# Kernel optimization log

Hardware: AMD Instinct MI355X
Metric: run time of the kernel (lower is better)

The kernel has to match this reference:

```python
import math
import jax, jax.numpy as jnp
import numpy as np
from jax import lax

B, T, D, H, F, K = 4, 1024, 512, 8, 2048, 31
DK = D // H


def _ln(x, g, b, eps=1e-5):
    m = jnp.mean(x, -1, keepdims=True)
    v = jnp.mean((x - m) ** 2, -1, keepdims=True)
    return (x - m) * lax.rsqrt(v + eps) * g + b


def setup_inputs():
    key = jax.random.key(0)
    ks = jax.random.split(key, 16)
    r = lambda k, s: (0.02 * jax.random.normal(k, s)).astype(jnp.float32)
    ones = lambda s: jnp.ones(s, jnp.float32)
    zeros = lambda s: jnp.zeros(s, jnp.float32)
    return {
        'x': jax.random.normal(ks[0], (B, T, D), jnp.float32),
        'pos_k': r(ks[1], (T, T, DK)),
        'mask': jnp.ones((B, T, T), jnp.int32),
        'ffn_in_ln_g': ones((D,)), 'ffn_in_ln_b': zeros((D,)),
        'ffn_in_w1': r(ks[2], (D, F)), 'ffn_in_b1': zeros((F,)),
        'ffn_in_w2': r(ks[3], (F, D)), 'ffn_in_b2': zeros((D,)),
        'attn_ln_g': ones((D,)), 'attn_ln_b': zeros((D,)),
        'wq': r(ks[4], (D, D)), 'bq': zeros((D,)),
        'wk': r(ks[5], (D, D)), 'bk': zeros((D,)),
        'wv': r(ks[6], (D, D)), 'bv': zeros((D,)),
        'wo': r(ks[7], (D, D)), 'bo': zeros((D,)),
        'conv_ln_g': ones((D,)), 'conv_ln_b': zeros((D,)),
        'pw1_w': jnp.asarray([1.0, 1.0], jnp.float32), 'pw1_b': zeros((2,)),
        'dw_w': r(ks[8], (D, 1, K)), 'dw_b': zeros((D,)),
        'pw2_w': jnp.asarray(1.0, jnp.float32), 'pw2_b': jnp.asarray(0.0, jnp.float32),
        'ffn_out_ln_g': ones((D,)), 'ffn_out_ln_b': zeros((D,)),
        'ffn_out_w1': r(ks[9], (D, F)), 'ffn_out_b1': zeros((F,)),
        'ffn_out_w2': r(ks[10], (F, D)), 'ffn_out_b2': zeros((D,)),
        'final_ln_g': ones((D,)), 'final_ln_b': zeros((D,)),
    }


def reference(x, pos_k, mask,
              ffn_in_ln_g, ffn_in_ln_b, ffn_in_w1, ffn_in_b1, ffn_in_w2, ffn_in_b2,
              attn_ln_g, attn_ln_b, wq, bq, wk, bk, wv, bv, wo, bo,
              conv_ln_g, conv_ln_b, pw1_w, pw1_b, dw_w, dw_b, pw2_w, pw2_b,
              ffn_out_ln_g, ffn_out_ln_b, ffn_out_w1, ffn_out_b1, ffn_out_w2, ffn_out_b2,
              final_ln_g, final_ln_b):
    def ffn(z, g, b, w1, b1, w2, b2):
        h = jax.nn.relu(_ln(z, g, b) @ w1 + b1)
        return h @ w2 + b2

    # macaron FFN (half residual)
    x = x + 0.5 * ffn(x, ffn_in_ln_g, ffn_in_ln_b, ffn_in_w1, ffn_in_b1, ffn_in_w2, ffn_in_b2)

    # relative-position multi-head attention (pre-LN)
    y = _ln(x, attn_ln_g, attn_ln_b)
    q = (y @ wq + bq).reshape(B, T, H, DK).transpose(0, 2, 1, 3)  # bhtd
    k = (y @ wk + bk).reshape(B, T, H, DK).transpose(0, 2, 1, 3)
    v = (y @ wv + bv).reshape(B, T, H, DK).transpose(0, 2, 1, 3)
    A = jnp.einsum('bhtd,bhsd->bhts', q, k)
    Bm = jnp.einsum('bhtd,tsd->bhts', q, pos_k)  # rel-pos term
    scores = (A + Bm) / math.sqrt(DK)
    inv = mask[:, None, :, :] == 0  # (B,1,T,T)
    neg = jnp.finfo(scores.dtype).min
    scores = jnp.where(inv, neg, scores)
    attn = jnp.where(inv, 0.0, jax.nn.softmax(scores, axis=-1))
    ctx = jnp.einsum('bhts,bhsd->bhtd', attn, v).transpose(0, 2, 1, 3).reshape(B, T, D)
    x = x + ctx @ wo + bo

    # conv module: LN -> pointwise(1->2) GLU -> depthwise conv1d -> ReLU -> pointwise(1->1)
    y = _ln(x, conv_ln_g, conv_ln_b)
    y = (pw1_w[0] * y + pw1_b[0]) * jax.nn.sigmoid(pw1_w[1] * y + pw1_b[1])
    y = y.transpose(0, 2, 1)  # (B, D, T)
    pad = (K - 1) // 2
    y = lax.conv_general_dilated(y, dw_w, (1,), [(pad, pad)],
                                 dimension_numbers=('NCH', 'OIH', 'NCH'),
                                 feature_group_count=D) + dw_b[None, :, None]
    y = jax.nn.relu(y).transpose(0, 2, 1)  # (B, T, D)
    x = x + pw2_w * y + pw2_b

    # output FFN (half residual) + final LN
    x = x + 0.5 * ffn(x, ffn_out_ln_g, ffn_out_ln_b, ffn_out_w1, ffn_out_b1, ffn_out_w2, ffn_out_b2)
    out = _ln(x, final_ln_g, final_ln_b)
    return (out, pos_k, mask)
```

## Files before the change

### kernel.cpp

```cpp
#include <hip/hip_runtime.h>
#include <math.h>

static constexpr int Bsz = 4, Tn = 1024, Dn = 512, Hn = 8, Fn = 2048, Kw = 31, Dk = 64;
static constexpr size_t N_OUT  = (size_t)Bsz * Tn * Dn;
static constexpr size_t N_POSK = (size_t)Tn * Tn * Dk;
static constexpr size_t N_MASK = (size_t)Bsz * Tn * Tn;

typedef __attribute__((ext_vector_type(8))) short bhalf8;
typedef __attribute__((ext_vector_type(4))) float f4;

__device__ __forceinline__ ushort f2b(float f) {
  uint b = __float_as_uint(f);
  uint r = (b + 0x7FFFu + ((b >> 16) & 1u)) >> 16;
  return (ushort)r;
}
__device__ __forceinline__ float b2f(ushort u) {
  return __uint_as_float((uint)u << 16);
}

typedef const __attribute__((address_space(1))) unsigned int* gp1_t;
typedef __attribute__((address_space(3))) unsigned int* lp3_t;
__device__ __forceinline__ void gload16(const void* g, void* l) {
  __builtin_amdgcn_global_load_lds((gp1_t)g, (lp3_t)l, 16, 0, 0);
}

template <int GLU, int BF>
__global__ __launch_bounds__(256) void ln_kernel(
    const float* __restrict__ x, const float* __restrict__ g,
    const float* __restrict__ b, float* __restrict__ yf,
    ushort* __restrict__ yb, const float* __restrict__ pw1w,
    const float* __restrict__ pw1b) {
  const int row = blockIdx.x;
  const float* xr = x + (size_t)row * Dn;
  const int tid = threadIdx.x, wid = tid >> 6, lane = tid & 63;

  __shared__ float red[4];
  __shared__ float bc[2];

  float v0 = xr[tid], v1 = xr[tid + 256];
  float s = v0 + v1;
#pragma unroll
  for (int off = 32; off; off >>= 1) s += __shfl_xor(s, off);
  if (lane == 0) red[wid] = s;
  __syncthreads();
  if (tid == 0) bc[0] = (red[0] + red[1] + red[2] + red[3]) * (1.0f / Dn);
  __syncthreads();
  const float m = bc[0];
  const float d0 = v0 - m, d1 = v1 - m;
  float s2 = d0 * d0 + d1 * d1;
#pragma unroll
  for (int off = 32; off; off >>= 1) s2 += __shfl_xor(s2, off);
  if (lane == 0) red[wid] = s2;
  __syncthreads();
  if (tid == 0)
    bc[1] = rsqrtf((red[0] + red[1] + red[2] + red[3]) * (1.0f / Dn) + 1e-5f);
  __syncthreads();
  const float r = bc[1];

  float o0 = d0 * r * g[tid] + b[tid];
  float o1 = d1 * r * g[tid + 256] + b[tid + 256];
  if (GLU) {
    const float w0 = pw1w[0], w1 = pw1w[1], c0 = pw1b[0], c1 = pw1b[1];
    o0 = (w0 * o0 + c0) * (1.0f / (1.0f + expf(-(w1 * o0 + c1))));
    o1 = (w0 * o1 + c0) * (1.0f / (1.0f + expf(-(w1 * o1 + c1))));
  }
  if (BF) {
    yb[(size_t)row * Dn + tid] = f2b(o0);
    yb[(size_t)row * Dn + tid + 256] = f2b(o1);
  } else {
    yf[(size_t)row * Dn + tid] = o0;
    yf[(size_t)row * Dn + tid + 256] = o1;
  }
}

__global__ __launch_bounds__(256) void wcvt_kernel(const float* __restrict__ W,
                                                   ushort* __restrict__ Wt,
                                                   int K, int N) {
  __shared__ float tile[32][33];
  const int n0 = blockIdx.x * 32, k0 = blockIdx.y * 32;
  const int tx = threadIdx.x & 31, ty = threadIdx.x >> 5;
#pragma unroll
  for (int i = 0; i < 4; ++i) {
    int k = ty + i * 8;
    tile[k][tx] = W[(size_t)(k0 + k) * N + n0 + tx];
  }
  __syncthreads();
#pragma unroll
  for (int i = 0; i < 4; ++i) {
    int r = ty + i * 8;
    Wt[(size_t)(n0 + r) * K + k0 + tx] = f2b(tile[tx][r]);
  }
}

template <int MODE, int BM, int BN>
__global__ __launch_bounds__(256) void mgemm_kernel(
    const ushort* __restrict__ A, const ushort* __restrict__ Bt,
    const float* __restrict__ bias, const float* __restrict__ res,
    float* __restrict__ C, ushort* __restrict__ Cb, int M, int N, int K) {
  constexpr int NFM = BM / 32;
  constexpr int NFN = BN / 32;
  __shared__ ushort As[BM * 64];
  __shared__ ushort Bs[BN * 64];
  const int bm = blockIdx.y * BM, bn = blockIdx.x * BN;
  const int tid = threadIdx.x;
  const int wid = tid >> 6, l = tid & 63;
  const int wm = wid >> 1, wn = wid & 1;
  const int l16 = l & 15, lhi = l >> 4;

  f4 acc[NFM][NFN] = {};

  for (int k0 = 0; k0 < K; k0 += 64) {
#pragma unroll
    for (int i = 0; i < BM * 8 / 256; ++i) {
      int slot = tid + i * 256;
      int row = slot >> 3, c8 = slot & 7;
      gload16(A + (size_t)(bm + row) * K + k0 + c8 * 8, &As[slot * 8]);
    }
#pragma unroll
    for (int i = 0; i < BN * 8 / 256; ++i) {
      int slot = tid + i * 256;
      int row = slot >> 3, c8 = slot & 7;
      gload16(Bt + (size_t)(bn + row) * K + k0 + c8 * 8, &Bs[slot * 8]);
    }
    __syncthreads();
#pragma unroll
    for (int ks = 0; ks < 2; ++ks) {
      bhalf8 a[NFM], b[NFN];
#pragma unroll
      for (int mi = 0; mi < NFM; ++mi)
        a[mi] = *(const bhalf8*)&As[(wm * (BM / 2) + mi * 16 + l16) * 64 +
                                    ks * 32 + lhi * 8];
#pragma unroll
      for (int ni = 0; ni < NFN; ++ni)
        b[ni] = *(const bhalf8*)&Bs[(wn * (BN / 2) + ni * 16 + l16) * 64 +
                                    ks * 32 + lhi * 8];
#pragma unroll
      for (int mi = 0; mi < NFM; ++mi)
#pragma unroll
        for (int ni = 0; ni < NFN; ++ni)
          acc[mi][ni] = __builtin_amdgcn_mfma_f32_16x16x32_bf16(
              a[mi], b[ni], acc[mi][ni], 0, 0, 0);
    }
    __syncthreads();
  }

#pragma unroll
  for (int mi = 0; mi < NFM; ++mi) {
#pragma unroll
    for (int ni = 0; ni < NFN; ++ni) {
      const int col = bn + wn * (BN / 2) + ni * 16 + l16;
      const float bv = bias[col];
#pragma unroll
      for (int r = 0; r < 4; ++r) {
        const int row = bm + wm * (BM / 2) + mi * 16 + lhi * 4 + r;
        float v = acc[mi][ni][r] + bv;
        const size_t off = (size_t)row * N + col;
        if (MODE == 0) {
          Cb[off] = f2b(fmaxf(v, 0.0f));
        } else if (MODE == 4) {
          Cb[off] = f2b(v);
        } else {
          if (MODE == 1) v = res[off] + 0.5f * v;
          if (MODE == 3) v = res[off] + v;
          C[off] = v;
        }
      }
    }
  }
}

template <int PASS>
__global__ __launch_bounds__(256) void bmm_kernel(const ushort* __restrict__ qbf,
                                                  const float* __restrict__ pk,
                                                  ushort* __restrict__ Sc16,
                                                  float* __restrict__ pkout) {
  const int s0 = blockIdx.x * 256;
  const int t = blockIdx.y;
  const int tid = threadIdx.x, wid = tid >> 6, l = tid & 63;
  const int l16 = l & 15, lhi = l >> 4;

  __shared__ ushort Qs[32 * 64];
  __shared__ ushort Ps[256 * 64];

  {
    int row = tid >> 3, c8 = tid & 7;
    int bq = row >> 3, hq = row & 7;
    *(uint4*)&Qs[row * 64 + c8 * 8] =
        *(const uint4*)(qbf + ((size_t)(bq * Tn + t)) * Dn + hq * 64 + c8 * 8);
  }
#pragma unroll
  for (int i = 0; i < 16; ++i) {
    int slot = tid + i * 256;
    int sr = slot >> 4, c4 = slot & 15;
    const size_t goff = ((size_t)t * Tn + s0 + sr) * Dk + c4 * 4;
    const float4 p = *(const float4*)(pk + goff);
    if (PASS) *(float4*)(pkout + goff) = p;
    ushort4 u;
    u.x = f2b(p.x);
    u.y = f2b(p.y);
    u.z = f2b(p.z);
    u.w = f2b(p.w);
    *(ushort4*)&Ps[sr * 64 + c4 * 4] = u;
  }
  __syncthreads();

  f4 acc[2][4] = {};
#pragma unroll
  for (int ks = 0; ks < 2; ++ks) {
    bhalf8 a[2], b[4];
#pragma unroll
    for (int mi = 0; mi < 2; ++mi)
      a[mi] = *(const bhalf8*)&Qs[(mi * 16 + l16) * 64 + ks * 32 + lhi * 8];
#pragma unroll
    for (int ni = 0; ni < 4; ++ni)
      b[ni] = *(const bhalf8*)&Ps[(wid * 64 + ni * 16 + l16) * 64 + ks * 32 +
                                  lhi * 8];
#pragma unroll
    for (int mi = 0; mi < 2; ++mi)
#pragma unroll
      for (int ni = 0; ni < 4; ++ni)
        acc[mi][ni] = __builtin_amdgcn_mfma_f32_16x16x32_bf16(
            a[mi], b[ni], acc[mi][ni], 0, 0, 0);
  }

  __syncthreads();
#pragma unroll
  for (int mi = 0; mi < 2; ++mi)
#pragma unroll
    for (int ni = 0; ni < 4; ++ni)
#pragma unroll
      for (int r = 0; r < 4; ++r) {
        const int bh = mi * 16 + lhi * 4 + r;
        const int sl = wid * 64 + ni * 16 + l16;
        Ps[bh * 256 + sl] = f2b(acc[mi][ni][r]);
      }
  __syncthreads();
#pragma unroll
  for (int i = 0; i < 4; ++i) {
    int idx = tid + i * 256;
    int bh = idx >> 5, sc = (idx & 31) * 8;
    *(uint4*)&Sc16[((size_t)bh * Tn + t) * Tn + s0 + sc] =
        *(const uint4*)&Ps[bh * 256 + sc];
  }
}

__global__ __launch_bounds__(256) void fattn_kernel(
    const ushort* __restrict__ qbf, const ushort* __restrict__ kbf,
    const ushort* __restrict__ vbf, const ushort* __restrict__ Sc16,
    const uint* __restrict__ mbits, ushort* __restrict__ ctxb) {
  const int bh = blockIdx.y;
  const int b = bh >> 3, h = bh & 7;
  const int t0 = blockIdx.x * 128;
  const int tid = threadIdx.x;
  const int wid = tid >> 6, l = tid & 63;
  const int l16 = l & 15, lhi = l >> 4;

  __shared__ ushort KV[8448];
  __shared__ ushort Ps[128 * 128];

  bhalf8 qa[2][2];
  {
#pragma unroll
    for (int i = 0; i < 4; ++i) {
      int slot = tid + i * 256;
      int row = slot >> 3, c8 = slot & 7;
      gload16(qbf + ((size_t)(b * Tn + t0 + row)) * Dn + h * 64 + c8 * 8,
              &Ps[slot * 8]);
    }
    __syncthreads();
#pragma unroll
    for (int mi = 0; mi < 2; ++mi)
#pragma unroll
      for (int ks = 0; ks < 2; ++ks)
        qa[mi][ks] = *(const bhalf8*)&Ps[(wid * 32 + mi * 16 + l16) * 64 +
                                         ks * 32 + lhi * 8];
    __syncthreads();
  }

  f4 oacc[2][4] = {};
  float mrow[2][4], lrow[2][4];
#pragma unroll
  for (int mi = 0; mi < 2; ++mi)
#pragma unroll
    for (int r = 0; r < 4; ++r) {
      mrow[mi][r] = -3.0e38f;
      lrow[mi][r] = 0.0f;
    }

  const float scale = 0.125f;
  for (int s0 = 0; s0 < Tn; s0 += 128) {
#pragma unroll
    for (int i = 0; i < 4; ++i) {
      int slot = tid + i * 256;
      int row = slot >> 3, c8 = slot & 7;
      gload16(kbf + ((size_t)(b * Tn + s0 + row)) * Dn + h * 64 + c8 * 8,
              &KV[slot * 8]);
    }
    f4 accs[2][8];
#pragma unroll
    for (int mi = 0; mi < 2; ++mi)
#pragma unroll
      for (int r = 0; r < 4; ++r) {
        const int trow = t0 + wid * 32 + mi * 16 + lhi * 4 + r;
        const ushort* src = Sc16 + ((size_t)bh * Tn + trow) * Tn + s0;
#pragma unroll
        for (int ni = 0; ni < 8; ++ni) accs[mi][ni][r] = b2f(src[ni * 16 + l16]);
      }
    __syncthreads();

#pragma unroll
    for (int ks = 0; ks < 2; ++ks) {
      bhalf8 bb[8];
#pragma unroll
      for (int ni = 0; ni < 8; ++ni)
        bb[ni] = *(const bhalf8*)&KV[(ni * 16 + l16) * 64 + ks * 32 + lhi * 8];
#pragma unroll
      for (int mi = 0; mi < 2; ++mi)
#pragma unroll
        for (int ni = 0; ni < 8; ++ni)
          accs[mi][ni] = __builtin_amdgcn_mfma_f32_16x16x32_bf16(
              qa[mi][ks], bb[ni], accs[mi][ni], 0, 0, 0);
    }

#pragma unroll
    for (int mi = 0; mi < 2; ++mi)
#pragma unroll
      for (int r = 0; r < 4; ++r) {
        const int trow = t0 + wid * 32 + mi * 16 + lhi * 4 + r;
        const uint* mw = mbits + ((size_t)b * Tn + trow) * 32 + (s0 >> 5);
        const uint w[4] = {mw[0], mw[1], mw[2], mw[3]};
        float p[8];
        float rm = -3.0e38f;
#pragma unroll
        for (int ni = 0; ni < 8; ++ni) {
          float v = accs[mi][ni][r] * scale;
          const uint bit = (w[ni >> 1] >> ((ni & 1) * 16 + l16)) & 1u;
          v = bit ? v : -3.0e38f;
          p[ni] = v;
          rm = fmaxf(rm, v);
        }
#pragma unroll
        for (int off = 8; off; off >>= 1) rm = fmaxf(rm, __shfl_xor(rm, off));
        const float mnew = fmaxf(mrow[mi][r], rm);
        const float sold = __expf(mrow[mi][r] - mnew);
        mrow[mi][r] = mnew;
        float rs = 0.0f;
#pragma unroll
        for (int ni = 0; ni < 8; ++ni) {
          const float e = __expf(p[ni] - mnew);
          rs += e;
          p[ni] = e;
        }
#pragma unroll
        for (int off = 8; off; off >>= 1) rs += __shfl_xor(rs, off);
        lrow[mi][r] = lrow[mi][r] * sold + rs;
#pragma unroll
        for (int ni = 0; ni < 4; ++ni) oacc[mi][ni][r] *= sold;
        const int lr = wid * 32 + mi * 16 + lhi * 4 + r;
#pragma unroll
        for (int ni = 0; ni < 8; ++ni) {
          const int byte =
              (lr * 256 + (ni * 16 + l16) * 2) ^ ((lr & 7) << 4);
          *(ushort*)((char*)Ps + byte) = f2b(p[ni]);
        }
      }
    __syncthreads();

#pragma unroll
    for (int i = 0; i < 4; ++i) {
      int slot = tid + i * 256;
      int sr = slot >> 3, c8 = slot & 7;
      const uint4 raw = *(const uint4*)(
          vbf + ((size_t)(b * Tn + s0 + sr)) * Dn + h * 64 + c8 * 8);
      const ushort* e = (const ushort*)&raw;
#pragma unroll
      for (int j = 0; j < 8; ++j) KV[(c8 * 8 + j) * 132 + sr] = e[j];
    }
    __syncthreads();

#pragma unroll
    for (int ks = 0; ks < 4; ++ks) {
      bhalf8 a[2], bb[4];
#pragma unroll
      for (int mi = 0; mi < 2; ++mi) {
        const int lr = wid * 32 + mi * 16 + l16;
        const int byte = (lr * 256 + ks * 64 + lhi * 16) ^ ((lr & 7) << 4);
        a[mi] = *(const bhalf8*)((char*)Ps + byte);
      }
#pragma unroll
      for (int ni = 0; ni < 4; ++ni)
        bb[ni] = *(const bhalf8*)&KV[(ni * 16 + l16) * 132 + ks * 32 + lhi * 8];
#pragma unroll
      for (int mi = 0; mi < 2; ++mi)
#pragma unroll
        for (int ni = 0; ni < 4; ++ni)
          oacc[mi][ni] = __builtin_amdgcn_mfma_f32_16x16x32_bf16(
              a[mi], bb[ni], oacc[mi][ni], 0, 0, 0);
    }
    __syncthreads();
  }

#pragma unroll
  for (int mi = 0; mi < 2; ++mi)
#pragma unroll
    for (int r = 0; r < 4; ++r) {
      const float inv = (mrow[mi][r] <= -1.0e37f)
                            ? 0.0f
                            : 1.0f / fmaxf(lrow[mi][r], 1e-30f);
      const int t = t0 + wid * 32 + mi * 16 + lhi * 4 + r;
#pragma unroll
      for (int ni = 0; ni < 4; ++ni) {
        const int d = ni * 16 + l16;
        ctxb[((size_t)(b * Tn + t)) * Dn + h * 64 + d] =
            f2b(oacc[mi][ni][r] * inv);
      }
    }
}

__global__ __launch_bounds__(256) void conv2_kernel(
    const float* __restrict__ y, const float* __restrict__ dww,
    const float* __restrict__ dwb, const float* __restrict__ pw2w,
    const float* __restrict__ pw2b, float* __restrict__ x) {
  const int b = blockIdx.z;
  const int d0 = blockIdx.y * 256;
  const int t0 = blockIdx.x * 16;
  const int tid = threadIdx.x;
  const int d = d0 + tid;

  __shared__ float wlds[256 * Kw];
#pragma unroll
  for (int i = 0; i < Kw; ++i)
    wlds[i * 256 + tid] = dww[(size_t)d0 * Kw + i * 256 + tid];
  __syncthreads();

  float w[Kw];
#pragma unroll
  for (int k = 0; k < Kw; ++k) w[k] = wlds[tid * Kw + k];

  float v[46];
#pragma unroll
  for (int i = 0; i < 46; ++i) {
    int t = t0 - 15 + i;
    v[i] = (t >= 0 && t < Tn) ? y[((size_t)b * Tn + t) * Dn + d] : 0.0f;
  }

  const float bias = dwb[d], w2 = pw2w[0], c2 = pw2b[0];
#pragma unroll
  for (int j = 0; j < 16; ++j) {
    float acc = bias;
#pragma unroll
    for (int k = 0; k < Kw; ++k) acc += w[k] * v[j + k];
    acc = fmaxf(acc, 0.0f);
    const size_t idx = ((size_t)b * Tn + t0 + j) * Dn + d;
    x[idx] = x[idx] + w2 * acc + c2;
  }
}

__global__ __launch_bounds__(256) void maskcvt_kernel(
    const int* __restrict__ in, float* __restrict__ outf,
    uint* __restrict__ mbits) {
  const size_t idx = (size_t)blockIdx.x * 256 + threadIdx.x;
  const size_t base = idx * 32;
  uint bits = 0;
#pragma unroll
  for (int j = 0; j < 8; ++j) {
    const int4 v = *(const int4*)(in + base + j * 4);
    float4 f;
    f.x = (float)v.x;
    f.y = (float)v.y;
    f.z = (float)v.z;
    f.w = (float)v.w;
    *(float4*)(outf + base + j * 4) = f;
    bits |= (v.x != 0 ? 1u : 0u) << (j * 4 + 0);
    bits |= (v.y != 0 ? 1u : 0u) << (j * 4 + 1);
    bits |= (v.z != 0 ? 1u : 0u) << (j * 4 + 2);
    bits |= (v.w != 0 ? 1u : 0u) << (j * 4 + 3);
  }
  mbits[idx] = bits;
}

extern "C" void kernel_launch(void* const* d_in, const int* in_sizes, int n_in,
                              void* d_out, int out_size, void* d_ws,
                              size_t ws_size, hipStream_t stream) {
  const float* x = (const float*)d_in[0];
  const float* pos_k = (const float*)d_in[1];
  const int* mask = (const int*)d_in[2];
  const float* fi_g = (const float*)d_in[3];
  const float* fi_b = (const float*)d_in[4];
  const float* fi_w1 = (const float*)d_in[5];
  const float* fi_b1 = (const float*)d_in[6];
  const float* fi_w2 = (const float*)d_in[7];
  const float* fi_b2 = (const float*)d_in[8];
  const float* at_g = (const float*)d_in[9];
  const float* at_b = (const float*)d_in[10];
  const float* wq = (const float*)d_in[11];
  const float* bq = (const float*)d_in[12];
  const float* wk = (const float*)d_in[13];
  const float* bk = (const float*)d_in[14];
  const float* wv = (const float*)d_in[15];
  const float* bv = (const float*)d_in[16];
  const float* wo = (const float*)d_in[17];
  const float* bo = (const float*)d_in[18];
  const float* cv_g = (const float*)d_in[19];
  const float* cv_b = (const float*)d_in[20];
  const float* pw1w = (const float*)d_in[21];
  const float* pw1b = (const float*)d_in[22];
  const float* dww = (const float*)d_in[23];
  const float* dwb = (const float*)d_in[24];
  const float* pw2w = (const float*)d_in[25];
  const float* pw2b = (const float*)d_in[26];
  const float* fo_g = (const float*)d_in[27];
  const float* fo_b = (const float*)d_in[28];
  const float* fo_w1 = (const float*)d_in[29];
  const float* fo_b1 = (const float*)d_in[30];
  const float* fo_w2 = (const float*)d_in[31];
  const float* fo_b2 = (const float*)d_in[32];
  const float* fl_g = (const float*)d_in[33];
  const float* fl_b = (const float*)d_in[34];

  float* out = (float*)d_out;

  float* xcur = (float*)d_ws;
  float* y = xcur + N_OUT;
  uint* mbits = (uint*)(y + N_OUT);

  const size_t NEED = (size_t)206 << 20;
  const bool fused = ws_size >= NEED;
  char* sp = fused ? (char*)(mbits + N_MASK / 32) : (char*)(out + N_OUT);
  auto alloc16 = [&](size_t elems) {
    ushort* p = (ushort*)sp;
    sp += ((elems * 2 + 255) & ~(size_t)255);
    return p;
  };
  ushort* Sc16 = alloc16((size_t)32 * Tn * Tn);
  ushort* wt_fi1 = alloc16((size_t)Fn * Dn);
  ushort* wt_fi2 = alloc16((size_t)Dn * Fn);
  ushort* wt_q = alloc16((size_t)Dn * Dn);
  ushort* wt_k = alloc16((size_t)Dn * Dn);
  ushort* wt_v = alloc16((size_t)Dn * Dn);
  ushort* wt_o = alloc16((size_t)Dn * Dn);
  ushort* wt_fo1 = alloc16((size_t)Fn * Dn);
  ushort* wt_fo2 = alloc16((size_t)Dn * Fn);
  ushort* ybf = alloc16(N_OUT);
  ushort* hbf = alloc16((size_t)Bsz * Tn * Fn);
  ushort* ctxbf = alloc16(N_OUT);
  ushort* qbf = alloc16(N_OUT);
  ushort* kbf = alloc16(N_OUT);
  ushort* vbf = alloc16(N_OUT);

  const int M = Bsz * Tn;
  const dim3 blk256(256);
  const dim3 grid_rows(M);
  const dim3 gF(Fn / 128, M / 128);
  const dim3 gD64(Dn / 64, M / 64);
  const dim3 gRect(Dn / 64, M / 128);

  hipMemcpyAsync(xcur, x, N_OUT * sizeof(float), hipMemcpyDeviceToDevice,
                 stream);

  maskcvt_kernel<<<dim3(N_MASK / 32 / 256), blk256, 0, stream>>>(
      mask, out + N_OUT + N_POSK, mbits);

  wcvt_kernel<<<dim3(Fn / 32, Dn / 32), blk256, 0, stream>>>(fi_w1, wt_fi1, Dn, Fn);
  wcvt_kernel<<<dim3(Dn / 32, Fn / 32), blk256, 0, stream>>>(fi_w2, wt_fi2, Fn, Dn);
  wcvt_kernel<<<dim3(Dn / 32, Dn / 32), blk256, 0, stream>>>(wq, wt_q, Dn, Dn);
  wcvt_kernel<<<dim3(Dn / 32, Dn / 32), blk256, 0, stream>>>(wk, wt_k, Dn, Dn);
  wcvt_kernel<<<dim3(Dn / 32, Dn / 32), blk256, 0, stream>>>(wv, wt_v, Dn, Dn);
  wcvt_kernel<<<dim3(Dn / 32, Dn / 32), blk256, 0, stream>>>(wo, wt_o, Dn, Dn);
  wcvt_kernel<<<dim3(Fn / 32, Dn / 32), blk256, 0, stream>>>(fo_w1, wt_fo1, Dn, Fn);
  wcvt_kernel<<<dim3(Dn / 32, Fn / 32), blk256, 0, stream>>>(fo_w2, wt_fo2, Fn, Dn);

  ln_kernel<0, 1><<<grid_rows, blk256, 0, stream>>>(xcur, fi_g, fi_b, nullptr,
                                                    ybf, nullptr, nullptr);
  mgemm_kernel<0, 128, 128><<<gF, blk256, 0, stream>>>(
      ybf, wt_fi1, fi_b1, nullptr, nullptr, hbf, M, Fn, Dn);
  mgemm_kernel<1, 128, 64><<<gRect, blk256, 0, stream>>>(
      hbf, wt_fi2, fi_b2, xcur, xcur, nullptr, M, Dn, Fn);

  ln_kernel<0, 1><<<grid_rows, blk256, 0, stream>>>(xcur, at_g, at_b, nullptr,
                                                    ybf, nullptr, nullptr);
  mgemm_kernel<4, 64, 64><<<gD64, blk256, 0, stream>>>(
      ybf, wt_q, bq, nullptr, nullptr, qbf, M, Dn, Dn);
  mgemm_kernel<4, 64, 64><<<gD64, blk256, 0, stream>>>(
      ybf, wt_k, bk, nullptr, nullptr, kbf, M, Dn, Dn);
  mgemm_kernel<4, 64, 64><<<gD64, blk256, 0, stream>>>(
      ybf, wt_v, bv, nullptr, nullptr, vbf, M, Dn, Dn);

  if (fused)
    bmm_kernel<1><<<dim3(4, Tn), blk256, 0, stream>>>(qbf, pos_k, Sc16,
                                                      out + N_OUT);
  else
    bmm_kernel<0><<<dim3(4, Tn), blk256, 0, stream>>>(qbf, pos_k, Sc16,
                                                      nullptr);

  fattn_kernel<<<dim3(Tn / 128, 32), blk256, 0, stream>>>(qbf, kbf, vbf, Sc16,
                                                          mbits, ctxbf);

  mgemm_kernel<3, 64, 64><<<gD64, blk256, 0, stream>>>(
      ctxbf, wt_o, bo, xcur, xcur, nullptr, M, Dn, Dn);

  ln_kernel<1, 0><<<grid_rows, blk256, 0, stream>>>(xcur, cv_g, cv_b, y,
                                                    nullptr, pw1w, pw1b);
  conv2_kernel<<<dim3(Tn / 16, 2, Bsz), blk256, 0, stream>>>(y, dww, dwb, pw2w,
                                                             pw2b, xcur);

  ln_kernel<0, 1><<<grid_rows, blk256, 0, stream>>>(xcur, fo_g, fo_b, nullptr,
                                                    ybf, nullptr, nullptr);
  mgemm_kernel<0, 128, 128><<<gF, blk256, 0, stream>>>(
      ybf, wt_fo1, fo_b1, nullptr, nullptr, hbf, M, Fn, Dn);
  mgemm_kernel<1, 128, 64><<<gRect, blk256, 0, stream>>>(
      hbf, wt_fo2, fo_b2, xcur, xcur, nullptr, M, Dn, Fn);

  ln_kernel<0, 0><<<grid_rows, blk256, 0, stream>>>(xcur, fl_g, fl_b, out,
                                                    nullptr, nullptr, nullptr);

  if (!fused)
    hipMemcpyAsync(out + N_OUT, pos_k, N_POSK * sizeof(float),
                   hipMemcpyDeviceToDevice, stream);
}
```

Baseline: 418.7 us.

## Fuse QKV projections, batch weight conversions, stage score tiles in LDS

The three Q/K/V GEMMs become one GEMM over a concatenated weight into an interleaved QKV buffer. The eight weight-conversion launches are merged into one kernel. The initial device copy of x is dropped by reading x directly in the first LN and residual. The attention kernel now stages the precomputed rel-pos score tile into swizzled LDS with async global-to-LDS loads instead of scattered 2-byte global reads. These cut launch count, bandwidth and uncoalesced loads, at the cost of a wider row stride for Q/K/V reads and an extra barrier before the score read.

```diff
diff --git a/kernel.cpp b/kernel.cpp
--- a/kernel.cpp
+++ b/kernel.cpp
@@ -2,6 +2,7 @@
 #include <math.h>
 
 static constexpr int Bsz = 4, Tn = 1024, Dn = 512, Hn = 8, Fn = 2048, Kw = 31, Dk = 64;
+static constexpr int QS = 3 * Dn;
 static constexpr size_t N_OUT  = (size_t)Bsz * Tn * Dn;
 static constexpr size_t N_POSK = (size_t)Tn * Tn * Dk;
 static constexpr size_t N_MASK = (size_t)Bsz * Tn * Tn;
@@ -73,29 +74,46 @@
   }
 }
 
-__global__ __launch_bounds__(256) void wcvt_kernel(const float* __restrict__ W,
-                                                   ushort* __restrict__ Wt,
-                                                   int K, int N) {
-  __shared__ float tile[32][33];
-  const int n0 = blockIdx.x * 32, k0 = blockIdx.y * 32;
+__global__ __launch_bounds__(256) void wcvt8_kernel(
+    const float* s0, const float* s1, const float* s2, const float* s3,
+    const float* s4, const float* s5, const float* s6, const float* s7,
+    ushort* d0, ushort* d1, ushort* d2, ushort* d3, ushort* d4, ushort* d5,
+    ushort* d6, ushort* d7) {
+  int bid = blockIdx.x;
+  const float* W;
+  ushort* Wt;
+  int K, N, tile;
+  if (bid < 1024)      { W = s0; Wt = d0; K = Dn; N = Fn; tile = bid; }
+  else if (bid < 2048) { W = s1; Wt = d1; K = Fn; N = Dn; tile = bid - 1024; }
+  else if (bid < 2304) { W = s2; Wt = d2; K = Dn; N = Dn; tile = bid - 2048; }
+  else if (bid < 2560) { W = s3; Wt = d3; K = Dn; N = Dn; tile = bid - 2304; }
+  else if (bid < 2816) { W = s4; Wt = d4; K = Dn; N = Dn; tile = bid - 2560; }
+  else if (bid < 3072) { W = s5; Wt = d5; K = Dn; N = Dn; tile = bid - 2816; }
+  else if (bid < 4096) { W = s6; Wt = d6; K = Dn; N = Fn; tile = bid - 3072; }
+  else                 { W = s7; Wt = d7; K = Fn; N = Dn; tile = bid - 4096; }
+  const int nt = N / 32;
+  const int n0 = (tile % nt) * 32, k0 = (tile / nt) * 32;
+
+  __shared__ float tilebuf[32][33];
   const int tx = threadIdx.x & 31, ty = threadIdx.x >> 5;
 #pragma unroll
   for (int i = 0; i < 4; ++i) {
     int k = ty + i * 8;
-    tile[k][tx] = W[(size_t)(k0 + k) * N + n0 + tx];
+    tilebuf[k][tx] = W[(size_t)(k0 + k) * N + n0 + tx];
   }
   __syncthreads();
 #pragma unroll
   for (int i = 0; i < 4; ++i) {
     int r = ty + i * 8;
-    Wt[(size_t)(n0 + r) * K + k0 + tx] = f2b(tile[tx][r]);
+    Wt[(size_t)(n0 + r) * K + k0 + tx] = f2b(tilebuf[tx][r]);
   }
 }
 
 template <int MODE, int BM, int BN>
 __global__ __launch_bounds__(256) void mgemm_kernel(
     const ushort* __restrict__ A, const ushort* __restrict__ Bt,
-    const float* __restrict__ bias, const float* __restrict__ res,
+    const float* __restrict__ bias, const float* __restrict__ bias2,
+    const float* __restrict__ bias3, const float* __restrict__ res,
     float* __restrict__ C, ushort* __restrict__ Cb, int M, int N, int K) {
   constexpr int NFM = BM / 32;
   constexpr int NFN = BN / 32;
@@ -149,7 +167,12 @@
 #pragma unroll
     for (int ni = 0; ni < NFN; ++ni) {
       const int col = bn + wn * (BN / 2) + ni * 16 + l16;
-      const float bv = bias[col];
+      float bv;
+      if (MODE == 4)
+        bv = col < 512 ? bias[col]
+                       : (col < 1024 ? bias2[col - 512] : bias3[col - 1024]);
+      else
+        bv = bias[col];
 #pragma unroll
       for (int r = 0; r < 4; ++r) {
         const int row = bm + wm * (BM / 2) + mi * 16 + lhi * 4 + r;
@@ -170,7 +193,7 @@
 }
 
 template <int PASS>
-__global__ __launch_bounds__(256) void bmm_kernel(const ushort* __restrict__ qbf,
+__global__ __launch_bounds__(256) void bmm_kernel(const ushort* __restrict__ qkv,
                                                   const float* __restrict__ pk,
                                                   ushort* __restrict__ Sc16,
                                                   float* __restrict__ pkout) {
@@ -185,8 +208,8 @@
   {
     int row = tid >> 3, c8 = tid & 7;
     int bq = row >> 3, hq = row & 7;
-    *(uint4*)&Qs[row * 64 + c8 * 8] =
-        *(const uint4*)(qbf + ((size_t)(bq * Tn + t)) * Dn + hq * 64 + c8 * 8);
+    *(uint4*)&Qs[row * 64 + c8 * 8] = *(const uint4*)(
+        qkv + ((size_t)(bq * Tn + t)) * QS + hq * 64 + c8 * 8);
   }
 #pragma unroll
   for (int i = 0; i < 16; ++i) {
@@ -245,8 +268,7 @@
 }
 
 __global__ __launch_bounds__(256) void fattn_kernel(
-    const ushort* __restrict__ qbf, const ushort* __restrict__ kbf,
-    const ushort* __restrict__ vbf, const ushort* __restrict__ Sc16,
+    const ushort* __restrict__ qkv, const ushort* __restrict__ Sc16,
     const uint* __restrict__ mbits, ushort* __restrict__ ctxb) {
   const int bh = blockIdx.y;
   const int b = bh >> 3, h = bh & 7;
@@ -264,7 +286,7 @@
     for (int i = 0; i < 4; ++i) {
       int slot = tid + i * 256;
       int row = slot >> 3, c8 = slot & 7;
-      gload16(qbf + ((size_t)(b * Tn + t0 + row)) * Dn + h * 64 + c8 * 8,
+      gload16(qkv + ((size_t)(b * Tn + t0 + row)) * QS + h * 64 + c8 * 8,
               &Ps[slot * 8]);
     }
     __syncthreads();
@@ -293,20 +315,32 @@
     for (int i = 0; i < 4; ++i) {
       int slot = tid + i * 256;
       int row = slot >> 3, c8 = slot & 7;
-      gload16(kbf + ((size_t)(b * Tn + s0 + row)) * Dn + h * 64 + c8 * 8,
+      gload16(qkv + ((size_t)(b * Tn + s0 + row)) * QS + 512 + h * 64 + c8 * 8,
               &KV[slot * 8]);
     }
+#pragma unroll
+    for (int i = 0; i < 8; ++i) {
+      int slot = tid + i * 256;
+      int row = slot >> 4, c16 = slot & 15;
+      int cb = (c16 * 16) ^ ((row & 7) << 4);
+      gload16(
+          (const char*)(Sc16 + ((size_t)bh * Tn + t0 + row) * Tn + s0) + cb,
+          (char*)Ps + slot * 16);
+    }
+    __syncthreads();
+
     f4 accs[2][8];
 #pragma unroll
     for (int mi = 0; mi < 2; ++mi)
 #pragma unroll
       for (int r = 0; r < 4; ++r) {
-        const int trow = t0 + wid * 32 + mi * 16 + lhi * 4 + r;
-        const ushort* src = Sc16 + ((size_t)bh * Tn + trow) * Tn + s0;
-#pragma unroll
-        for (int ni = 0; ni < 8; ++ni) accs[mi][ni][r] = b2f(src[ni * 16 + l16]);
+        const int lr = wid * 32 + mi * 16 + lhi * 4 + r;
+#pragma unroll
+        for (int ni = 0; ni < 8; ++ni) {
+          const int cb = ((ni * 16 + l16) * 2) ^ ((lr & 7) << 4);
+          accs[mi][ni][r] = b2f(*(const ushort*)((const char*)Ps + lr * 256 + cb));
+        }
       }
-    __syncthreads();
 
 #pragma unroll
     for (int ks = 0; ks < 2; ++ks) {
@@ -360,7 +394,7 @@
 #pragma unroll
         for (int ni = 0; ni < 8; ++ni) {
           const int byte =
-              (lr * 256 + (ni * 16 + l16) * 2) ^ ((lr & 7) << 4);
+              (lr * 256 + (((ni * 16 + l16) * 2) ^ ((lr & 7) << 4)));
           *(ushort*)((char*)Ps + byte) = f2b(p[ni]);
         }
       }
@@ -371,7 +405,7 @@
       int slot = tid + i * 256;
       int sr = slot >> 3, c8 = slot & 7;
       const uint4 raw = *(const uint4*)(
-          vbf + ((size_t)(b * Tn + s0 + sr)) * Dn + h * 64 + c8 * 8);
+          qkv + ((size_t)(b * Tn + s0 + sr)) * QS + 1024 + h * 64 + c8 * 8);
       const ushort* e = (const ushort*)&raw;
 #pragma unroll
       for (int j = 0; j < 8; ++j) KV[(c8 * 8 + j) * 132 + sr] = e[j];
@@ -384,7 +418,7 @@
 #pragma unroll
       for (int mi = 0; mi < 2; ++mi) {
         const int lr = wid * 32 + mi * 16 + l16;
-        const int byte = (lr * 256 + ks * 64 + lhi * 16) ^ ((lr & 7) << 4);
+        const int byte = (lr * 256 + ((ks * 64 + lhi * 16) ^ ((lr & 7) << 4)));
         a[mi] = *(const bhalf8*)((char*)Ps + byte);
       }
 #pragma unroll
@@ -535,18 +569,14 @@
   ushort* Sc16 = alloc16((size_t)32 * Tn * Tn);
   ushort* wt_fi1 = alloc16((size_t)Fn * Dn);
   ushort* wt_fi2 = alloc16((size_t)Dn * Fn);
-  ushort* wt_q = alloc16((size_t)Dn * Dn);
-  ushort* wt_k = alloc16((size_t)Dn * Dn);
-  ushort* wt_v = alloc16((size_t)Dn * Dn);
+  ushort* wt_qkv = alloc16((size_t)QS * Dn);
   ushort* wt_o = alloc16((size_t)Dn * Dn);
   ushort* wt_fo1 = alloc16((size_t)Fn * Dn);
   ushort* wt_fo2 = alloc16((size_t)Dn * Fn);
   ushort* ybf = alloc16(N_OUT);
   ushort* hbf = alloc16((size_t)Bsz * Tn * Fn);
   ushort* ctxbf = alloc16(N_OUT);
-  ushort* qbf = alloc16(N_OUT);
-  ushort* kbf = alloc16(N_OUT);
-  ushort* vbf = alloc16(N_OUT);
+  ushort* qkvbf = alloc16((size_t)Bsz * Tn * QS);
 
   const int M = Bsz * Tn;
   const dim3 blk256(256);
@@ -554,50 +584,40 @@
   const dim3 gF(Fn / 128, M / 128);
   const dim3 gD64(Dn / 64, M / 64);
   const dim3 gRect(Dn / 64, M / 128);
-
-  hipMemcpyAsync(xcur, x, N_OUT * sizeof(float), hipMemcpyDeviceToDevice,
-                 stream);
+  const dim3 gQKV(QS / 64, M / 128);
 
   maskcvt_kernel<<<dim3(N_MASK / 32 / 256), blk256, 0, stream>>>(
       mask, out + N_OUT + N_POSK, mbits);
 
-  wcvt_kernel<<<dim3(Fn / 32, Dn / 32), blk256, 0, stream>>>(fi_w1, wt_fi1, Dn, Fn);
-  wcvt_kernel<<<dim3(Dn / 32, Fn / 32), blk256, 0, stream>>>(fi_w2, wt_fi2, Fn, Dn);
-  wcvt_kernel<<<dim3(Dn / 32, Dn / 32), blk256, 0, stream>>>(wq, wt_q, Dn, Dn);
-  wcvt_kernel<<<dim3(Dn / 32, Dn / 32), blk256, 0, stream>>>(wk, wt_k, Dn, Dn);
-  wcvt_kernel<<<dim3(Dn / 32, Dn / 32), blk256, 0, stream>>>(wv, wt_v, Dn, Dn);
-  wcvt_kernel<<<dim3(Dn / 32, Dn / 32), blk256, 0, stream>>>(wo, wt_o, Dn, Dn);
-  wcvt_kernel<<<dim3(Fn / 32, Dn / 32), blk256, 0, stream>>>(fo_w1, wt_fo1, Dn, Fn);
-  wcvt_kernel<<<dim3(Dn / 32, Fn / 32), blk256, 0, stream>>>(fo_w2, wt_fo2, Fn, Dn);
-
-  ln_kernel<0, 1><<<grid_rows, blk256, 0, stream>>>(xcur, fi_g, fi_b, nullptr,
+  wcvt8_kernel<<<dim3(5120), blk256, 0, stream>>>(
+      fi_w1, fi_w2, wq, wk, wv, wo, fo_w1, fo_w2, wt_fi1, wt_fi2, wt_qkv,
+      wt_qkv + (size_t)Dn * Dn, wt_qkv + (size_t)2 * Dn * Dn, wt_o, wt_fo1,
+      wt_fo2);
+
+  ln_kernel<0, 1><<<grid_rows, blk256, 0, stream>>>(x, fi_g, fi_b, nullptr,
                                                     ybf, nullptr, nullptr);
   mgemm_kernel<0, 128, 128><<<gF, blk256, 0, stream>>>(
-      ybf, wt_fi1, fi_b1, nullptr, nullptr, hbf, M, Fn, Dn);
+      ybf, wt_fi1, fi_b1, nullptr, nullptr, nullptr, nullptr, hbf, M, Fn, Dn);
   mgemm_kernel<1, 128, 64><<<gRect, blk256, 0, stream>>>(
-      hbf, wt_fi2, fi_b2, xcur, xcur, nullptr, M, Dn, Fn);
+      hbf, wt_fi2, fi_b2, nullptr, nullptr, x, xcur, nullptr, M, Dn, Fn);
 
   ln_kernel<0, 1><<<grid_rows, blk256, 0, stream>>>(xcur, at_g, at_b, nullptr,
                                                     ybf, nullptr, nullptr);
-  mgemm_kernel<4, 64, 64><<<gD64, blk256, 0, stream>>>(
-      ybf, wt_q, bq, nullptr, nullptr, qbf, M, Dn, Dn);
-  mgemm_kernel<4, 64, 64><<<gD64, blk256, 0, stream>>>(
-      ybf, wt_k, bk, nullptr, nullptr, kbf, M, Dn, Dn);
-  mgemm_kernel<4, 64, 64><<<gD64, blk256, 0, stream>>>(
-      ybf, wt_v, bv, nullptr, nullptr, vbf, M, Dn, Dn);
+  mgemm_kernel<4, 128, 64><<<gQKV, blk256, 0, stream>>>(
+      ybf, wt_qkv, bq, bk, bv, nullptr, nullptr, qkvbf, M, QS, Dn);
 
   if (fused)
-    bmm_kernel<1><<<dim3(4, Tn), blk256, 0, stream>>>(qbf, pos_k, Sc16,
+    bmm_kernel<1><<<dim3(4, Tn), blk256, 0, stream>>>(qkvbf, pos_k, Sc16,
                                                       out + N_OUT);
   else
-    bmm_kernel<0><<<dim3(4, Tn), blk256, 0, stream>>>(qbf, pos_k, Sc16,
+    bmm_kernel<0><<<dim3(4, Tn), blk256, 0, stream>>>(qkvbf, pos_k, Sc16,
                                                       nullptr);
 
-  fattn_kernel<<<dim3(Tn / 128, 32), blk256, 0, stream>>>(qbf, kbf, vbf, Sc16,
-                                                          mbits, ctxbf);
+  fattn_kernel<<<dim3(Tn / 128, 32), blk256, 0, stream>>>(qkvbf, Sc16, mbits,
+                                                          ctxbf);
 
   mgemm_kernel<3, 64, 64><<<gD64, blk256, 0, stream>>>(
-      ctxbf, wt_o, bo, xcur, xcur, nullptr, M, Dn, Dn);
+      ctxbf, wt_o, bo, nullptr, nullptr, xcur, xcur, nullptr, M, Dn, Dn);
 
   ln_kernel<1, 0><<<grid_rows, blk256, 0, stream>>>(xcur, cv_g, cv_b, y,
                                                     nullptr, pw1w, pw1b);
@@ -607,9 +627,9 @@
   ln_kernel<0, 1><<<grid_rows, blk256, 0, stream>>>(xcur, fo_g, fo_b, nullptr,
                                                     ybf, nullptr, nullptr);
   mgemm_kernel<0, 128, 128><<<gF, blk256, 0, stream>>>(
-      ybf, wt_fo1, fo_b1, nullptr, nullptr, hbf, M, Fn, Dn);
+      ybf, wt_fo1, fo_b1, nullptr, nullptr, nullptr, nullptr, hbf, M, Fn, Dn);
   mgemm_kernel<1, 128, 64><<<gRect, blk256, 0, stream>>>(
-      hbf, wt_fo2, fo_b2, xcur, xcur, nullptr, M, Dn, Fn);
+      hbf, wt_fo2, fo_b2, nullptr, nullptr, xcur, xcur, nullptr, M, Dn, Fn);
 
   ln_kernel<0, 0><<<grid_rows, blk256, 0, stream>>>(xcur, fl_g, fl_b, out,
                                                     nullptr, nullptr, nullptr);
```

New measurement: 389.4 us. 7.0% less time.
